# Performance work log

Hardware: AMD Instinct MI355X
Metric: run time of the kernel (lower is better)

Reference implementation:

```python
import jax, jax.numpy as jnp
import numpy as np

N = 4096        # n_locations
D_MODEL = 512
H, D_K, D_V = 4, 128, 256


def setup_inputs() -> dict:
    key = jax.random.key(0)
    ks = jax.random.split(key, 7)
    s = 0.02
    return {
        "Q": jax.random.normal(ks[0], (N, D_MODEL), dtype=jnp.float32),
        "K": jax.random.normal(ks[1], (N, D_MODEL), dtype=jnp.float32),
        "V": jax.random.normal(ks[2], (N, D_MODEL), dtype=jnp.float32),
        "Wq": jax.random.normal(ks[3], (H, D_MODEL, D_K), dtype=jnp.float32) * s,
        "Wk": jax.random.normal(ks[4], (H, D_MODEL, D_K), dtype=jnp.float32) * s,
        "Wv": jax.random.normal(ks[5], (H, D_MODEL, D_V), dtype=jnp.float32) * s,
        "Wo": jax.random.normal(ks[6], (D_MODEL, H * D_V), dtype=jnp.float32) * s,
    }


def reference(Q, K, V, Wq, Wk, Wv, Wo):
    n = K.shape[0]
    # Batched per-head projections: [h, n, d_k] / [h, n, d_v]
    q = jnp.einsum('nd,hdk->hnk', Q, Wq)
    k = jnp.einsum('nd,hdk->hnk', K, Wk)
    v = jnp.einsum('nd,hdv->hnv', V, Wv)
    # NOTE: original scales by sqrt(n_locations) (K.size(0)), not sqrt(d_k)
    scores = jnp.einsum('hqk,hnk->hqn', q, k) / jnp.sqrt(jnp.asarray(n, q.dtype))
    weights = jax.nn.softmax(scores, axis=-1)          # [h, n, n]
    heads = jnp.einsum('hqn,hnv->hqv', weights, v)      # [h, n, d_v]
    # concat heads along feature dim: [n, h*d_v]
    x = jnp.transpose(heads, (1, 0, 2)).reshape(heads.shape[1], -1)
    return x @ Wo.T                                     # [n, d_model]
```

## Files before the change

kernel.cpp:

```cpp
#include <hip/hip_runtime.h>
#include <hip/hip_bf16.h>
#include <type_traits>

typedef __hip_bfloat16 bf16;
typedef __attribute__((ext_vector_type(8))) short bf16x8;
typedef __attribute__((ext_vector_type(4))) float f32x4;

#define N_LOC 4096
#define DMODEL 512
#define NHEAD 4
#define DK 128
#define DV 256

__device__ __forceinline__ bf16 to_bf16(float f) { return __float2bfloat16(f); }

__device__ __forceinline__ void dma16(const bf16* g, bf16* l) {
  __builtin_amdgcn_global_load_lds((const __attribute__((address_space(1))) unsigned int*)g,
                                   (__attribute__((address_space(3))) unsigned int*)l, 16, 0, 0);
}

__global__ __launch_bounds__(256) void convert_all(const float* __restrict__ Q,
                                                   const float* __restrict__ K,
                                                   const float* __restrict__ V,
                                                   const float* __restrict__ Wo,
                                                   bf16* __restrict__ Qb, bf16* __restrict__ Kb,
                                                   bf16* __restrict__ Vb, bf16* __restrict__ Wob) {
  long i = ((long)blockIdx.x * 256 + threadIdx.x) * 8;
  const float* src;
  bf16* dst;
  long off;
  if (i < 2097152)      { src = Q;  dst = Qb;  off = i; }
  else if (i < 4194304) { src = K;  dst = Kb;  off = i - 2097152; }
  else if (i < 6291456) { src = V;  dst = Vb;  off = i - 4194304; }
  else                  { src = Wo; dst = Wob; off = i - 6291456; }
  float4 a = *(const float4*)&src[off];
  float4 b = *(const float4*)&src[off + 4];
  union { bf16 h[8]; bf16x8 v; } u;
  u.h[0] = to_bf16(a.x); u.h[1] = to_bf16(a.y); u.h[2] = to_bf16(a.z); u.h[3] = to_bf16(a.w);
  u.h[4] = to_bf16(b.x); u.h[5] = to_bf16(b.y); u.h[6] = to_bf16(b.z); u.h[7] = to_bf16(b.w);
  *(bf16x8*)&dst[off] = u.v;
}

__global__ __launch_bounds__(256) void pack_wt(const float* __restrict__ Wq,
                                               const float* __restrict__ Wk,
                                               const float* __restrict__ Wv,
                                               bf16* __restrict__ oq, bf16* __restrict__ ok,
                                               bf16* __restrict__ ov) {
  int z = blockIdx.z;
  const float* W = (z == 0) ? Wq : (z == 1) ? Wk : Wv;
  bf16* out = (z == 0) ? oq : (z == 1) ? ok : ov;
  int DH = (z == 2) ? 256 : 128;
  int nt = DH >> 6;
  int y = blockIdx.y;
  if (y >= 4 * nt) return;
  int h = y / nt, tt = y - h * nt;
  int d0 = blockIdx.x * 64, t0 = tt * 64;
  __shared__ float tile[64][65];
  for (int i = threadIdx.x; i < 4096; i += 256) {
    int r = i >> 6, c = i & 63;
    tile[r][c] = W[((size_t)h * 512 + d0 + r) * DH + t0 + c];
  }
  __syncthreads();
  for (int i = threadIdx.x; i < 4096; i += 256) {
    int t = i >> 6, d = i & 63;
    out[((size_t)(h * DH + t0 + t)) * 512 + d0 + d] = to_bf16(tile[d][t]);
  }
}

template <typename OutT>
__global__ __launch_bounds__(256) void gemm_bt(const bf16* __restrict__ A,
                                               const bf16* __restrict__ Bt,
                                               OutT* __restrict__ C, int M, int N, int K) {
  const int LD = 72;
  __shared__ bf16 As[64 * LD];
  __shared__ bf16 Bs[64 * LD];
  int tid = threadIdx.x;
  int lane = tid & 63, w = tid >> 6;
  int quad = lane >> 4, l16 = lane & 15;
  int wm = (w >> 1) * 32, wn = (w & 1) * 32;
  int m0 = blockIdx.x * 64, n0 = blockIdx.y * 64;

  f32x4 acc[2][2] = {};
  for (int k0 = 0; k0 < K; k0 += 64) {
    for (int i = tid; i < 64 * 8; i += 256) {
      int r = i >> 3, c = (i & 7) * 8;
      *(bf16x8*)&As[r * LD + c] = *(const bf16x8*)&A[(long)(m0 + r) * K + k0 + c];
      *(bf16x8*)&Bs[r * LD + c] = *(const bf16x8*)&Bt[(long)(n0 + r) * K + k0 + c];
    }
    __syncthreads();
#pragma unroll
    for (int kk = 0; kk < 2; kk++) {
      bf16x8 af[2], bfr[2];
#pragma unroll
      for (int i = 0; i < 2; i++)
        af[i] = *(const bf16x8*)&As[(wm + i * 16 + l16) * LD + kk * 32 + quad * 8];
#pragma unroll
      for (int j = 0; j < 2; j++)
        bfr[j] = *(const bf16x8*)&Bs[(wn + j * 16 + l16) * LD + kk * 32 + quad * 8];
#pragma unroll
      for (int i = 0; i < 2; i++)
#pragma unroll
        for (int j = 0; j < 2; j++)
          acc[i][j] = __builtin_amdgcn_mfma_f32_16x16x32_bf16(af[i], bfr[j], acc[i][j], 0, 0, 0);
    }
    __syncthreads();
  }
#pragma unroll
  for (int i = 0; i < 2; i++)
#pragma unroll
    for (int j = 0; j < 2; j++)
#pragma unroll
      for (int r = 0; r < 4; r++) {
        long row = m0 + wm + i * 16 + quad * 4 + r;
        long col = n0 + wn + j * 16 + l16;
        if constexpr (std::is_same<OutT, bf16>::value)
          C[row * N + col] = to_bf16(acc[i][j][r]);
        else
          C[row * N + col] = acc[i][j][r];
      }
}

__global__ __launch_bounds__(256) void transpose_bf16(const bf16* __restrict__ in,
                                                      bf16* __restrict__ out, int R, int Cc) {
  __shared__ bf16 t[64][65];
  int r0 = blockIdx.x * 64, c0 = blockIdx.y * 64;
  for (int i = threadIdx.x; i < 64 * 64; i += 256) {
    int r = i >> 6, c = i & 63;
    t[r][c] = in[(long)(r0 + r) * Cc + c0 + c];
  }
  __syncthreads();
  for (int i = threadIdx.x; i < 64 * 64; i += 256) {
    int c = i >> 6, r = i & 63;
    out[(long)(c0 + c) * R + r0 + r] = t[r][c];
  }
}

__global__ __launch_bounds__(512, 4) void attn(const bf16* __restrict__ qb,
                                               const bf16* __restrict__ kb,
                                               const bf16* __restrict__ vT,
                                               bf16* __restrict__ x) {
  __shared__ __align__(16) bf16 kt[64 * 128];
  __shared__ __align__(16) bf16 vt[256 * 64];
  __shared__ __align__(16) bf16 pt[64 * 72];
  __shared__ float Lrow[64];

  const int head = blockIdx.x & 3;
  const int q0 = (blockIdx.x >> 2) * 64;
  const int tid = threadIdx.x;
  const int lane = tid & 63, w = tid >> 6;
  const int quad = lane >> 4, l16 = lane & 15;
  const int cd = w & 3;
  const int g = w >> 2;

  bf16x8 onesf;
  {
    union { bf16 h[8]; bf16x8 v; } u;
    bf16 one = to_bf16(1.0f), zero = to_bf16(0.0f);
#pragma unroll
    for (int j = 0; j < 8; j++) u.h[j] = (l16 == 0) ? one : zero;
    onesf = u.v;
  }

  bf16x8 qf[2][4];
#pragma unroll
  for (int i = 0; i < 2; i++) {
    const bf16* qrow = &qb[(size_t)(q0 + g * 32 + i * 16 + l16) * 512 + head * 128];
#pragma unroll
    for (int kk = 0; kk < 4; kk++) qf[i][kk] = *(const bf16x8*)&qrow[kk * 32 + quad * 8];
  }

  f32x4 oacc[2][4] = {};
  f32x4 oL[2] = {};
  const float scale = 1.0f / 64.0f;

  for (int key0 = 0; key0 < N_LOC; key0 += 64) {
#pragma unroll
    for (int t2 = 0; t2 < 2; t2++) {
      int j = 2 * w + t2;
      int r = 4 * j + (lane >> 4);
      int p = lane & 15;
      int G = (p & 8) | ((p ^ r) & 7);
      dma16(&kb[(size_t)(key0 + r) * 512 + head * 128 + G * 8], &kt[j * 512]);
    }
#pragma unroll
    for (int t2 = 0; t2 < 4; t2++) {
      int j = 4 * w + t2;
      int r = 8 * j + (lane >> 3);
      int p = lane & 7;
      int G = (p ^ r) & 7;
      dma16(&vT[(size_t)(head * 256 + r) * 4096 + key0 + G * 8], &vt[j * 512]);
    }
    __syncthreads();

    f32x4 sacc[2] = {};
#pragma unroll
    for (int kk = 0; kk < 4; kk++) {
      int R = cd * 16 + l16;
      int G = kk * 4 + quad;
      bf16x8 kf = *(const bf16x8*)&kt[R * 128 + (((G ^ R) & 7) | (G & 8)) * 8];
      sacc[0] = __builtin_amdgcn_mfma_f32_16x16x32_bf16(qf[0][kk], kf, sacc[0], 0, 0, 0);
      sacc[1] = __builtin_amdgcn_mfma_f32_16x16x32_bf16(qf[1][kk], kf, sacc[1], 0, 0, 0);
    }
#pragma unroll
    for (int i = 0; i < 2; i++)
#pragma unroll
      for (int r = 0; r < 4; r++)
        pt[(g * 32 + i * 16 + quad * 4 + r) * 72 + cd * 16 + l16] =
            to_bf16(__expf(sacc[i][r] * scale));
    __syncthreads();

#pragma unroll
    for (int kk = 0; kk < 2; kk++) {
      bf16x8 pf[2];
#pragma unroll
      for (int i = 0; i < 2; i++)
        pf[i] = *(const bf16x8*)&pt[(g * 32 + i * 16 + l16) * 72 + kk * 32 + quad * 8];
#pragma unroll
      for (int c = 0; c < 4; c++) {
        int R = cd * 64 + c * 16 + l16;
        int G = kk * 4 + quad;
        bf16x8 vf = *(const bf16x8*)&vt[R * 64 + ((G ^ R) & 7) * 8];
#pragma unroll
        for (int i = 0; i < 2; i++)
          oacc[i][c] = __builtin_amdgcn_mfma_f32_16x16x32_bf16(pf[i], vf, oacc[i][c], 0, 0, 0);
      }
      if (cd == 3) {
#pragma unroll
        for (int i = 0; i < 2; i++)
          oL[i] = __builtin_amdgcn_mfma_f32_16x16x32_bf16(pf[i], onesf, oL[i], 0, 0, 0);
      }
    }
    __syncthreads();
  }

  if (cd == 3 && l16 == 0) {
#pragma unroll
    for (int i = 0; i < 2; i++)
#pragma unroll
      for (int r = 0; r < 4; r++) Lrow[g * 32 + i * 16 + quad * 4 + r] = oL[i][r];
  }
  __syncthreads();

#pragma unroll
  for (int i = 0; i < 2; i++)
#pragma unroll
    for (int c = 0; c < 4; c++)
#pragma unroll
      for (int r = 0; r < 4; r++) {
        int row = g * 32 + i * 16 + quad * 4 + r;
        float v = oacc[i][c][r] / Lrow[row];
        x[(size_t)(q0 + row) * 1024 + head * 256 + cd * 64 + c * 16 + l16] = to_bf16(v);
      }
}

extern "C" void kernel_launch(void* const* d_in, const int* in_sizes, int n_in,
                              void* d_out, int out_size, void* d_ws, size_t ws_size,
                              hipStream_t stream) {
  const float* Q  = (const float*)d_in[0];
  const float* Km = (const float*)d_in[1];
  const float* V  = (const float*)d_in[2];
  const float* Wq = (const float*)d_in[3];
  const float* Wk = (const float*)d_in[4];
  const float* Wv = (const float*)d_in[5];
  const float* Wo = (const float*)d_in[6];
  float* out = (float*)d_out;

  bf16* ws  = (bf16*)d_ws;
  bf16* Qb  = ws;
  bf16* Kb  = Qb + 2097152;
  bf16* Vb  = Kb + 2097152;
  bf16* Wqt = Vb + 2097152;
  bf16* Wkt = Wqt + 262144;
  bf16* Wvt = Wkt + 262144;
  bf16* Wob = Wvt + 524288;
  bf16* qb  = Wob + 524288;
  bf16* kb  = qb + 2097152;
  bf16* vb  = kb + 2097152;
  bf16* vT  = vb + 4194304;
  bf16* x   = vT + 4194304;

  convert_all<<<3328, 256, 0, stream>>>(Q, Km, V, Wo, Qb, Kb, Vb, Wob);
  pack_wt<<<dim3(8, 16, 3), 256, 0, stream>>>(Wq, Wk, Wv, Wqt, Wkt, Wvt);

  gemm_bt<bf16><<<dim3(64, 8), 256, 0, stream>>>(Qb, Wqt, qb, 4096, 512, 512);
  gemm_bt<bf16><<<dim3(64, 8), 256, 0, stream>>>(Kb, Wkt, kb, 4096, 512, 512);
  gemm_bt<bf16><<<dim3(64, 16), 256, 0, stream>>>(Vb, Wvt, vb, 4096, 1024, 512);
  transpose_bf16<<<dim3(64, 16), 256, 0, stream>>>(vb, vT, 4096, 1024);

  attn<<<256, 512, 0, stream>>>(qb, kb, vT, x);

  gemm_bt<float><<<dim3(64, 8), 256, 0, stream>>>(x, Wob, out, 4096, 512, 1024);
}
```

Measured before the change: 249.7 us.

## Double-buffer attention K/V tiles, enlarge GEMM tiles, fuse projections, vectorize transpose

The attention kernel now double-buffers the K and V tiles in LDS. It prefetches the next key block with async global-to-LDS loads while computing the current one, and replaces __syncthreads with explicit waitcnt and barriers. Occupancy is lowered to 2 blocks per CU. The GEMMs move to 128x128 tiles with swizzled DMA loads into LDS, and the three projection GEMMs merge into one launch. The V transpose now uses 8x8 register blocks. The aim is to hide load latency and cut launch and LDS overhead, at the cost of more LDS and register pressure.

```diff
diff --git a/kernel.cpp b/kernel.cpp
--- a/kernel.cpp
+++ b/kernel.cpp
@@ -7,10 +7,6 @@
 typedef __attribute__((ext_vector_type(4))) float f32x4;
 
 #define N_LOC 4096
-#define DMODEL 512
-#define NHEAD 4
-#define DK 128
-#define DV 256
 
 __device__ __forceinline__ bf16 to_bf16(float f) { return __float2bfloat16(f); }
 
@@ -68,47 +64,51 @@
 }
 
 template <typename OutT>
-__global__ __launch_bounds__(256) void gemm_bt(const bf16* __restrict__ A,
-                                               const bf16* __restrict__ Bt,
-                                               OutT* __restrict__ C, int M, int N, int K) {
-  const int LD = 72;
-  __shared__ bf16 As[64 * LD];
-  __shared__ bf16 Bs[64 * LD];
+__device__ __forceinline__ void gemm128_body(const bf16* __restrict__ A,
+                                             const bf16* __restrict__ Bt,
+                                             OutT* __restrict__ C, int M, int N, int K,
+                                             int m0, int n0, bf16* As, bf16* Bs) {
   int tid = threadIdx.x;
   int lane = tid & 63, w = tid >> 6;
   int quad = lane >> 4, l16 = lane & 15;
-  int wm = (w >> 1) * 32, wn = (w & 1) * 32;
-  int m0 = blockIdx.x * 64, n0 = blockIdx.y * 64;
-
-  f32x4 acc[2][2] = {};
+  int wm = (w >> 1) * 64, wn = (w & 1) * 64;
+  int srow = lane >> 3;
+  int sG = (lane & 7) ^ srow;
+
+  f32x4 acc[4][4] = {};
   for (int k0 = 0; k0 < K; k0 += 64) {
-    for (int i = tid; i < 64 * 8; i += 256) {
-      int r = i >> 3, c = (i & 7) * 8;
-      *(bf16x8*)&As[r * LD + c] = *(const bf16x8*)&A[(long)(m0 + r) * K + k0 + c];
-      *(bf16x8*)&Bs[r * LD + c] = *(const bf16x8*)&Bt[(long)(n0 + r) * K + k0 + c];
+#pragma unroll
+    for (int j = 0; j < 4; j++) {
+      int rg = 4 * j + w;
+      dma16(&A[(long)(m0 + rg * 8 + srow) * K + k0 + sG * 8], &As[rg * 512]);
+      dma16(&Bt[(long)(n0 + rg * 8 + srow) * K + k0 + sG * 8], &Bs[rg * 512]);
     }
     __syncthreads();
 #pragma unroll
     for (int kk = 0; kk < 2; kk++) {
-      bf16x8 af[2], bfr[2];
-#pragma unroll
-      for (int i = 0; i < 2; i++)
-        af[i] = *(const bf16x8*)&As[(wm + i * 16 + l16) * LD + kk * 32 + quad * 8];
-#pragma unroll
-      for (int j = 0; j < 2; j++)
-        bfr[j] = *(const bf16x8*)&Bs[(wn + j * 16 + l16) * LD + kk * 32 + quad * 8];
-#pragma unroll
-      for (int i = 0; i < 2; i++)
-#pragma unroll
-        for (int j = 0; j < 2; j++)
+      bf16x8 af[4], bfr[4];
+#pragma unroll
+      for (int i = 0; i < 4; i++) {
+        int r = wm + i * 16 + l16;
+        af[i] = *(const bf16x8*)&As[r * 64 + (((kk * 4 + quad) ^ r) & 7) * 8];
+      }
+#pragma unroll
+      for (int j = 0; j < 4; j++) {
+        int r = wn + j * 16 + l16;
+        bfr[j] = *(const bf16x8*)&Bs[r * 64 + (((kk * 4 + quad) ^ r) & 7) * 8];
+      }
+#pragma unroll
+      for (int i = 0; i < 4; i++)
+#pragma unroll
+        for (int j = 0; j < 4; j++)
           acc[i][j] = __builtin_amdgcn_mfma_f32_16x16x32_bf16(af[i], bfr[j], acc[i][j], 0, 0, 0);
     }
     __syncthreads();
   }
 #pragma unroll
-  for (int i = 0; i < 2; i++)
-#pragma unroll
-    for (int j = 0; j < 2; j++)
+  for (int i = 0; i < 4; i++)
+#pragma unroll
+    for (int j = 0; j < 4; j++)
 #pragma unroll
       for (int r = 0; r < 4; r++) {
         long row = m0 + wm + i * 16 + quad * 4 + r;
@@ -120,27 +120,51 @@
       }
 }
 
+__global__ __launch_bounds__(256) void proj_gemm(const bf16* __restrict__ QKVb,
+                                                 const bf16* __restrict__ Wt,
+                                                 bf16* __restrict__ Cout) {
+  int z = blockIdx.z;
+  int N = (z == 2) ? 1024 : 512;
+  if ((int)(blockIdx.y * 128) >= N) return;
+  __shared__ __align__(16) bf16 As[128 * 64];
+  __shared__ __align__(16) bf16 Bs[128 * 64];
+  const bf16* A = QKVb + (size_t)z * 2097152;
+  const bf16* Bt = Wt + ((z == 2) ? (size_t)524288 : (size_t)z * 262144);
+  bf16* C = Cout + (size_t)z * 2097152;
+  gemm128_body<bf16>(A, Bt, C, 4096, N, 512, blockIdx.x * 128, blockIdx.y * 128, As, Bs);
+}
+
+__global__ __launch_bounds__(256) void out_gemm(const bf16* __restrict__ xin,
+                                                const bf16* __restrict__ Wob,
+                                                float* __restrict__ outp) {
+  __shared__ __align__(16) bf16 As[128 * 64];
+  __shared__ __align__(16) bf16 Bs[128 * 64];
+  gemm128_body<float>(xin, Wob, outp, 4096, 512, 1024, blockIdx.x * 128, blockIdx.y * 128, As, Bs);
+}
+
 __global__ __launch_bounds__(256) void transpose_bf16(const bf16* __restrict__ in,
                                                       bf16* __restrict__ out, int R, int Cc) {
-  __shared__ bf16 t[64][65];
-  int r0 = blockIdx.x * 64, c0 = blockIdx.y * 64;
-  for (int i = threadIdx.x; i < 64 * 64; i += 256) {
-    int r = i >> 6, c = i & 63;
-    t[r][c] = in[(long)(r0 + r) * Cc + c0 + c];
-  }
-  __syncthreads();
-  for (int i = threadIdx.x; i < 64 * 64; i += 256) {
-    int c = i >> 6, r = i & 63;
-    out[(long)(c0 + c) * R + r0 + r] = t[r][c];
-  }
-}
-
-__global__ __launch_bounds__(512, 4) void attn(const bf16* __restrict__ qb,
+  long T = (long)blockIdx.x * 256 + threadIdx.x;
+  long nrb = (long)(R >> 3);
+  long rb = T % nrb;
+  long cb = T / nrb;
+  union { bf16 h[8]; bf16x8 v; } a[8], b[8];
+#pragma unroll
+  for (int i = 0; i < 8; i++) a[i].v = *(const bf16x8*)&in[(rb * 8 + i) * Cc + cb * 8];
+#pragma unroll
+  for (int j = 0; j < 8; j++) {
+#pragma unroll
+    for (int i = 0; i < 8; i++) b[j].h[i] = a[i].h[j];
+    *(bf16x8*)&out[(cb * 8 + j) * R + rb * 8] = b[j].v;
+  }
+}
+
+__global__ __launch_bounds__(512, 2) void attn(const bf16* __restrict__ qb,
                                                const bf16* __restrict__ kb,
                                                const bf16* __restrict__ vT,
                                                bf16* __restrict__ x) {
-  __shared__ __align__(16) bf16 kt[64 * 128];
-  __shared__ __align__(16) bf16 vt[256 * 64];
+  __shared__ __align__(16) bf16 kt[2][64 * 128];
+  __shared__ __align__(16) bf16 vt[2][256 * 64];
   __shared__ __align__(16) bf16 pt[64 * 72];
   __shared__ float Lrow[64];
 
@@ -173,14 +197,14 @@
   f32x4 oL[2] = {};
   const float scale = 1.0f / 64.0f;
 
-  for (int key0 = 0; key0 < N_LOC; key0 += 64) {
+  auto stage = [&](int b, int key0) {
 #pragma unroll
     for (int t2 = 0; t2 < 2; t2++) {
       int j = 2 * w + t2;
       int r = 4 * j + (lane >> 4);
       int p = lane & 15;
       int G = (p & 8) | ((p ^ r) & 7);
-      dma16(&kb[(size_t)(key0 + r) * 512 + head * 128 + G * 8], &kt[j * 512]);
+      dma16(&kb[(size_t)(key0 + r) * 512 + head * 128 + G * 8], &kt[b][j * 512]);
     }
 #pragma unroll
     for (int t2 = 0; t2 < 4; t2++) {
@@ -188,16 +212,31 @@
       int r = 8 * j + (lane >> 3);
       int p = lane & 7;
       int G = (p ^ r) & 7;
-      dma16(&vT[(size_t)(head * 256 + r) * 4096 + key0 + G * 8], &vt[j * 512]);
-    }
-    __syncthreads();
-
+      dma16(&vT[(size_t)(head * 256 + r) * 4096 + key0 + G * 8], &vt[b][j * 512]);
+    }
+  };
+
+  stage(0, 0);
+  asm volatile("" ::: "memory");
+  int cur = 0;
+
+  for (int t = 0; t < 64; ++t) {
+    if (t < 63) {
+      stage(cur ^ 1, (t + 1) * 64);
+      asm volatile("s_waitcnt vmcnt(6)" ::: "memory");
+    } else {
+      asm volatile("s_waitcnt vmcnt(0)" ::: "memory");
+    }
+    __builtin_amdgcn_s_barrier();
+    asm volatile("" ::: "memory");
+
+    const bf16* ktc = kt[cur];
     f32x4 sacc[2] = {};
 #pragma unroll
     for (int kk = 0; kk < 4; kk++) {
       int R = cd * 16 + l16;
       int G = kk * 4 + quad;
-      bf16x8 kf = *(const bf16x8*)&kt[R * 128 + (((G ^ R) & 7) | (G & 8)) * 8];
+      bf16x8 kf = *(const bf16x8*)&ktc[R * 128 + (((G ^ R) & 7) | (G & 8)) * 8];
       sacc[0] = __builtin_amdgcn_mfma_f32_16x16x32_bf16(qf[0][kk], kf, sacc[0], 0, 0, 0);
       sacc[1] = __builtin_amdgcn_mfma_f32_16x16x32_bf16(qf[1][kk], kf, sacc[1], 0, 0, 0);
     }
@@ -207,8 +246,11 @@
       for (int r = 0; r < 4; r++)
         pt[(g * 32 + i * 16 + quad * 4 + r) * 72 + cd * 16 + l16] =
             to_bf16(__expf(sacc[i][r] * scale));
-    __syncthreads();
-
+    asm volatile("s_waitcnt lgkmcnt(0)" ::: "memory");
+    __builtin_amdgcn_s_barrier();
+    asm volatile("" ::: "memory");
+
+    const bf16* vtc = vt[cur];
 #pragma unroll
     for (int kk = 0; kk < 2; kk++) {
       bf16x8 pf[2];
@@ -219,7 +261,7 @@
       for (int c = 0; c < 4; c++) {
         int R = cd * 64 + c * 16 + l16;
         int G = kk * 4 + quad;
-        bf16x8 vf = *(const bf16x8*)&vt[R * 64 + ((G ^ R) & 7) * 8];
+        bf16x8 vf = *(const bf16x8*)&vtc[R * 64 + ((G ^ R) & 7) * 8];
 #pragma unroll
         for (int i = 0; i < 2; i++)
           oacc[i][c] = __builtin_amdgcn_mfma_f32_16x16x32_bf16(pf[i], vf, oacc[i][c], 0, 0, 0);
@@ -230,7 +272,10 @@
           oL[i] = __builtin_amdgcn_mfma_f32_16x16x32_bf16(pf[i], onesf, oL[i], 0, 0, 0);
       }
     }
-    __syncthreads();
+    asm volatile("" ::: "memory");
+    __builtin_amdgcn_s_barrier();
+    asm volatile("" ::: "memory");
+    cur ^= 1;
   }
 
   if (cd == 3 && l16 == 0) {
@@ -282,12 +327,10 @@
   convert_all<<<3328, 256, 0, stream>>>(Q, Km, V, Wo, Qb, Kb, Vb, Wob);
   pack_wt<<<dim3(8, 16, 3), 256, 0, stream>>>(Wq, Wk, Wv, Wqt, Wkt, Wvt);
 
-  gemm_bt<bf16><<<dim3(64, 8), 256, 0, stream>>>(Qb, Wqt, qb, 4096, 512, 512);
-  gemm_bt<bf16><<<dim3(64, 8), 256, 0, stream>>>(Kb, Wkt, kb, 4096, 512, 512);
-  gemm_bt<bf16><<<dim3(64, 16), 256, 0, stream>>>(Vb, Wvt, vb, 4096, 1024, 512);
-  transpose_bf16<<<dim3(64, 16), 256, 0, stream>>>(vb, vT, 4096, 1024);
+  proj_gemm<<<dim3(32, 8, 3), 256, 0, stream>>>(Qb, Wqt, qb);
+  transpose_bf16<<<256, 256, 0, stream>>>(vb, vT, 4096, 1024);
 
   attn<<<256, 512, 0, stream>>>(qb, kb, vT, x);
 
-  gemm_bt<float><<<dim3(64, 8), 256, 0, stream>>>(x, Wob, out, 4096, 512, 1024);
-}
+  out_gemm<<<dim3(32, 4), 256, 0, stream>>>(x, Wob, out);
+}
```

Result: faster. 227.8 us (-8.8%).
